# Kernel tuning notes

Measured on AMD Instinct MI355X. Metric: run time of the kernel, lower is better.

Reference implementation:

```python
import jax, jax.numpy as jnp
import numpy as np

T, D, H, E, K = 8192, 1024, 768, 16, 2


def setup_inputs() -> dict:
    key = jax.random.key(0)
    k1, k2, k3, k4, k5, k6 = jax.random.split(key, 6)
    x = jax.random.normal(k1, (T, D), dtype=jnp.float32)
    weights = jax.random.uniform(k2, (T, K), dtype=jnp.float32)
    indices = jax.random.randint(k3, (T, K), 0, E, dtype=jnp.int64)
    counts = jax.random.randint(k4, (E,), 0, 1024, dtype=jnp.int32)
    # GatedMLP params per expert: fc1: D -> 2H (value | gate), fc2: H -> D, no bias
    W1 = jax.random.normal(k5, (E, D, 2 * H), dtype=jnp.float32) * (1.0 / np.sqrt(D))
    W2 = jax.random.normal(k6, (E, H, D), dtype=jnp.float32) * (1.0 / np.sqrt(H))
    return {"x": x, "weights": weights, "indices": indices, "counts": counts, "W1": W1, "W2": W2}


def _gated_mlp(x, w1, w2):
    h = x @ w1                      # [T, 2H]
    v, g = jnp.split(h, 2, axis=-1)  # value, gate halves (torch chunk order)
    return (v * jax.nn.silu(g)) @ w2  # [T, D]


def reference(x, weights, indices, counts, W1, W2):
    # y[t] = sum_k weights[t,k] * GatedMLP_{indices[t,k]}(x[t])
    # Expressed as a masked per-expert combine: w_e[t] = sum_k weights[t,k]*[indices[t,k]==e].
    # Identical math to the torch gather/scatter loop (zero weight -> zero contribution).
    n_experts = W1.shape[0]
    y = jnp.zeros_like(x)
    for e in range(n_experts):
        w_e = jnp.sum(weights * (indices == e), axis=-1)  # [T]
        y = y + _gated_mlp(x, W1[e], W2[e]) * w_e[:, None]
    return y
```

## Files before the change

kernel.cpp:

```cpp
#include <hip/hip_runtime.h>
#include <hip/hip_bf16.h>

#define T_TOK 8192
#define D_DIM 1024
#define H_DIM 768
#define E_EXP 16
#define K_TOP 2
#define TK (T_TOK * K_TOP)
#define NT128 144
#define NT256 80

typedef __bf16 bf16x8 __attribute__((ext_vector_type(8)));
typedef unsigned short u16x8 __attribute__((ext_vector_type(8)));
typedef float f32x4 __attribute__((ext_vector_type(4)));

typedef const __attribute__((address_space(1))) void* gas_t;
typedef __attribute__((address_space(3))) void* las_t;

__device__ __forceinline__ unsigned short f2b(float f) {
    __hip_bfloat16 h = __float2bfloat16(f);
    return __builtin_bit_cast(unsigned short, h);
}
__device__ __forceinline__ float b2f(unsigned short u) {
    unsigned int x = ((unsigned int)u) << 16;
    return __builtin_bit_cast(float, x);
}

__global__ __launch_bounds__(1024) void k_route(
    const int* __restrict__ idx, const float* __restrict__ wts,
    int* __restrict__ offs, int* __restrict__ tiletab,
    int* __restrict__ rows, float* __restrict__ wslot, int* __restrict__ slot_of) {
    __shared__ int lcnt[E_EXP];
    __shared__ int lcur[E_EXP];
    const int tid = threadIdx.x;
    if (tid < E_EXP) lcnt[tid] = 0;
    __syncthreads();
    for (int i = tid; i < TK; i += 1024) atomicAdd(&lcnt[idx[i]], 1);
    __syncthreads();
    if (tid == 0) {
        int s = 0, nt = 0;
        for (int e = 0; e < E_EXP; ++e) {
            offs[e] = s;
            lcur[e] = s;
            const int n = lcnt[e];
            for (int m0 = 0; m0 < n; m0 += 128) tiletab[nt++] = (e << 16) | (m0 >> 7);
            s += n;
        }
        offs[E_EXP] = s;
        for (int i = nt; i < NT128; ++i) tiletab[i] = -1;
    }
    __syncthreads();
    for (int i = tid; i < TK; i += 1024) {
        const int e = idx[i];
        const int p = atomicAdd(&lcur[e], 1);
        rows[p] = i >> 1;
        wslot[p] = wts[i];
        slot_of[i] = p;
    }
}

#define PREP_X T_TOK
#define PREP_W1 (PREP_X + (D_DIM / 64) * ((2 * H_DIM) / 64) * E_EXP)
#define PREP_W2 (PREP_W1 + (H_DIM / 64) * (D_DIM / 64) * E_EXP)

__global__ __launch_bounds__(256) void k_prep(
    const float* __restrict__ x, const float* __restrict__ W1, const float* __restrict__ W2,
    unsigned short* __restrict__ xb, unsigned short* __restrict__ W1T,
    unsigned short* __restrict__ W2T) {
    const int b = blockIdx.x;
    const int tid = threadIdx.x;
    if (b < PREP_X) {
        const int d = tid * 4;
        const float4 v = *reinterpret_cast<const float4*>(&x[(size_t)b * D_DIM + d]);
        ushort4 u;
        u.x = f2b(v.x); u.y = f2b(v.y); u.z = f2b(v.z); u.w = f2b(v.w);
        *reinterpret_cast<ushort4*>(&xb[(size_t)b * D_DIM + d]) = u;
        return;
    }
    __shared__ float t4[64][65];
    const float* src; unsigned short* dst; int K, C, e, kb, cb, pack;
    if (b < PREP_W1) {
        const int q = b - PREP_X;
        K = D_DIM; C = 2 * H_DIM; pack = 1;
        e = q / ((K / 64) * (C / 64));
        const int r = q % ((K / 64) * (C / 64));
        kb = (r % (K / 64)) * 64; cb = (r / (K / 64)) * 64;
        src = W1; dst = W1T;
    } else {
        const int q = b - PREP_W1;
        K = H_DIM; C = D_DIM; pack = 0;
        e = q / ((K / 64) * (C / 64));
        const int r = q % ((K / 64) * (C / 64));
        kb = (r % (K / 64)) * 64; cb = (r / (K / 64)) * 64;
        src = W2; dst = W2T;
    }
    const float* s = src + ((size_t)e * K + kb) * C + cb;
#pragma unroll
    for (int i = 0; i < 4; ++i) {
        const int kk = (tid >> 4) + i * 16, c4 = (tid & 15) * 4;
        const float4 v = *reinterpret_cast<const float4*>(&s[(size_t)kk * C + c4]);
        t4[kk][c4] = v.x; t4[kk][c4 + 1] = v.y; t4[kk][c4 + 2] = v.z; t4[kk][c4 + 3] = v.w;
    }
    __syncthreads();
#pragma unroll
    for (int i = 0; i < 4; ++i) {
        const int cc = (tid >> 4) + i * 16, k4 = (tid & 15) * 4;
        const int j = cb + cc;
        int drow;
        if (pack) drow = (j < H_DIM) ? ((j >> 5) * 64 + (j & 31))
                                     : (((j - H_DIM) >> 5) * 64 + 32 + ((j - H_DIM) & 31));
        else drow = j;
        ushort4 u;
        u.x = f2b(t4[k4][cc]); u.y = f2b(t4[k4 + 1][cc]);
        u.z = f2b(t4[k4 + 2][cc]); u.w = f2b(t4[k4 + 3][cc]);
        *reinterpret_cast<ushort4*>(&dst[((size_t)e * C + drow) * K + kb + k4]) = u;
    }
}


__global__ __launch_bounds__(512, 2) void k_gemm1_fast(
    const unsigned short* __restrict__ xb, const unsigned short* __restrict__ W1T,
    const int* __restrict__ offs, const int* __restrict__ tiletab,
    const int* __restrict__ rows, unsigned short* __restrict__ act) {
    const int ti = (blockIdx.x & 7) * (NT128 / 8) + (blockIdx.x >> 3);
    const int tt = tiletab[ti];
    if (tt < 0) return;
    const int e = tt >> 16, m0 = (tt & 0xffff) << 7;
    const int off = offs[e], n_e = offs[e + 1] - off;
    const int by = blockIdx.y;

    __shared__ unsigned short SA[2][128 * 32];
    __shared__ unsigned short SB[2][256 * 32];

    const int tid = threadIdx.x;
    const int wid = tid >> 6, lane = tid & 63;
    const int l15 = lane & 15, kq = lane >> 4;
    const int wm = wid >> 2, wn = wid & 3;
    const int srow = tid >> 2;
    const int esw = (((tid & 3) ^ ((tid >> 3) & 3)) << 3);
    const int rk = ((kq ^ ((l15 >> 1) & 3)) << 3);

    int tok;
    { int s = m0 + srow; s = (s < n_e) ? s : (n_e - 1); tok = rows[off + s]; }
    size_t bB[2];
#pragma unroll
    for (int j = 0; j < 2; ++j)
        bB[j] = ((size_t)e * (2 * H_DIM) + by * 256 + j * 128 + srow) * D_DIM + esw;

    f32x4 acc[4][4];
#pragma unroll
    for (int m = 0; m < 4; ++m)
#pragma unroll
        for (int n = 0; n < 4; ++n)
#pragma unroll
            for (int r = 0; r < 4; ++r) acc[m][n][r] = 0.f;

    auto stage = [&](int buf, int k0) {
        const unsigned short* ga = xb + (size_t)tok * D_DIM + k0 + esw;
        __builtin_amdgcn_global_load_lds((gas_t)ga,
            (las_t)((char*)&SA[buf][0] + tid * 16), 16, 0, 0);
#pragma unroll
        for (int j = 0; j < 2; ++j) {
            const unsigned short* gb = W1T + bB[j] + k0;
            __builtin_amdgcn_global_load_lds((gas_t)gb,
                (las_t)((char*)&SB[buf][0] + j * 8192 + tid * 16), 16, 0, 0);
        }
    };

    stage(0, 0);
    __syncthreads();
    int c = 0;
    const int NT = D_DIM / 32;
    for (int t = 0; t < NT; ++t) {
        if (t + 1 < NT) stage(c ^ 1, (t + 1) * 32);
        bf16x8 a[4], b[4];
#pragma unroll
        for (int m = 0; m < 4; ++m) {
            const int row = wm * 64 + m * 16 + l15;
            a[m] = __builtin_bit_cast(bf16x8, *reinterpret_cast<const u16x8*>(
                &SA[c][row * 32 + rk]));
        }
#pragma unroll
        for (int n = 0; n < 4; ++n) {
            const int row = wn * 64 + n * 16 + l15;
            b[n] = __builtin_bit_cast(bf16x8, *reinterpret_cast<const u16x8*>(
                &SB[c][row * 32 + rk]));
        }
#pragma unroll
        for (int m = 0; m < 4; ++m)
#pragma unroll
            for (int n = 0; n < 4; ++n)
                acc[m][n] = __builtin_amdgcn_mfma_f32_16x16x32_bf16(a[m], b[n], acc[m][n], 0, 0, 0);
        __syncthreads();
        c ^= 1;
    }
#pragma unroll
    for (int m = 0; m < 4; ++m)
#pragma unroll
        for (int r = 0; r < 4; ++r) {
            const int row = wm * 64 + m * 16 + kq * 4 + r;
            if (m0 + row < n_e) {
#pragma unroll
                for (int nv = 0; nv < 2; ++nv) {
                    const int col = by * 128 + wn * 32 + nv * 16 + l15;
                    const float vv = acc[m][nv][r], gg = acc[m][2 + nv][r];
                    const float s = gg / (1.0f + __expf(-gg));
                    act[(size_t)(off + m0 + row) * H_DIM + col] = f2b(vv * s);
                }
            }
        }
}

__global__ __launch_bounds__(512, 2) void k_gemm2_fast(
    const unsigned short* __restrict__ act, const unsigned short* __restrict__ W2T,
    const int* __restrict__ offs, const int* __restrict__ tiletab,
    const float* __restrict__ wslot, unsigned short* __restrict__ slot_out) {
    const int ti = (blockIdx.x & 7) * (NT128 / 8) + (blockIdx.x >> 3);
    const int tt = tiletab[ti];
    if (tt < 0) return;
    const int e = tt >> 16, m0 = (tt & 0xffff) << 7;
    const int off = offs[e], n_e = offs[e + 1] - off;
    const int by = blockIdx.y;

    __shared__ unsigned short SA[2][128 * 32];
    __shared__ unsigned short SB[2][256 * 32];

    const int tid = threadIdx.x;
    const int wid = tid >> 6, lane = tid & 63;
    const int l15 = lane & 15, kq = lane >> 4;
    const int wm = wid >> 2, wn = wid & 3;
    const int srow = tid >> 2;
    const int esw = (((tid & 3) ^ ((tid >> 3) & 3)) << 3);
    const int rk = ((kq ^ ((l15 >> 1) & 3)) << 3);

    int slotA;
    { int s = m0 + srow; s = (s < n_e) ? s : (n_e - 1); slotA = off + s; }
    size_t bB[2];
#pragma unroll
    for (int j = 0; j < 2; ++j)
        bB[j] = ((size_t)e * D_DIM + by * 256 + j * 128 + srow) * H_DIM + esw;

    f32x4 acc[4][4];
#pragma unroll
    for (int m = 0; m < 4; ++m)
#pragma unroll
        for (int n = 0; n < 4; ++n)
#pragma unroll
            for (int r = 0; r < 4; ++r) acc[m][n][r] = 0.f;

    auto stage = [&](int buf, int k0) {
        const unsigned short* ga = act + (size_t)slotA * H_DIM + k0 + esw;
        __builtin_amdgcn_global_load_lds((gas_t)ga,
            (las_t)((char*)&SA[buf][0] + tid * 16), 16, 0, 0);
#pragma unroll
        for (int j = 0; j < 2; ++j) {
            const unsigned short* gb = W2T + bB[j] + k0;
            __builtin_amdgcn_global_load_lds((gas_t)gb,
                (las_t)((char*)&SB[buf][0] + j * 8192 + tid * 16), 16, 0, 0);
        }
    };

    stage(0, 0);
    __syncthreads();
    int c = 0;
    const int NT = H_DIM / 32;
    for (int t = 0; t < NT; ++t) {
        if (t + 1 < NT) stage(c ^ 1, (t + 1) * 32);
        bf16x8 a[4], b[4];
#pragma unroll
        for (int m = 0; m < 4; ++m) {
            const int row = wm * 64 + m * 16 + l15;
            a[m] = __builtin_bit_cast(bf16x8, *reinterpret_cast<const u16x8*>(
                &SA[c][row * 32 + rk]));
        }
#pragma unroll
        for (int n = 0; n < 4; ++n) {
            const int row = wn * 64 + n * 16 + l15;
            b[n] = __builtin_bit_cast(bf16x8, *reinterpret_cast<const u16x8*>(
                &SB[c][row * 32 + rk]));
        }
#pragma unroll
        for (int m = 0; m < 4; ++m)
#pragma unroll
            for (int n = 0; n < 4; ++n)
                acc[m][n] = __builtin_amdgcn_mfma_f32_16x16x32_bf16(a[m], b[n], acc[m][n], 0, 0, 0);
        __syncthreads();
        c ^= 1;
    }
#pragma unroll
    for (int m = 0; m < 4; ++m)
#pragma unroll
        for (int r = 0; r < 4; ++r) {
            const int row = wm * 64 + m * 16 + kq * 4 + r;
            if (m0 + row < n_e) {
                const int slot = off + m0 + row;
                const float w = wslot[slot];
#pragma unroll
                for (int n = 0; n < 4; ++n) {
                    const int col = by * 256 + wn * 64 + n * 16 + l15;
                    slot_out[(size_t)slot * D_DIM + col] = f2b(w * acc[m][n][r]);
                }
            }
        }
}

__global__ __launch_bounds__(256) void k_gather(const float* __restrict__ x,
                                                const int* __restrict__ rows,
                                                unsigned short* __restrict__ xg) {
    const int s = blockIdx.x, t = threadIdx.x;
    const int tok = rows[s];
    const float4 v = *reinterpret_cast<const float4*>(&x[(size_t)tok * D_DIM + t * 4]);
    ushort4 u;
    u.x = f2b(v.x); u.y = f2b(v.y); u.z = f2b(v.z); u.w = f2b(v.w);
    *reinterpret_cast<ushort4*>(&xg[(size_t)s * D_DIM + t * 4]) = u;
}

__global__ __launch_bounds__(256) void k_gemm1_fb(
    const unsigned short* __restrict__ xg, const float* __restrict__ W1,
    const int* __restrict__ offs, const int* __restrict__ tiletab,
    unsigned short* __restrict__ act) {
    const int tt = tiletab[blockIdx.x];
    if (tt < 0) return;
    const int e = tt >> 16, m0 = (tt & 0xffff) << 7;
    const int off = offs[e], n_e = offs[e + 1] - off;
    const int h0 = blockIdx.y * 64;

    __shared__ unsigned short Ab[128 * 64];
    __shared__ unsigned short Bb[128 * 66];

    const int tid = threadIdx.x;
    const int wid = tid >> 6, lane = tid & 63;
    const int l15 = lane & 15, kq = lane >> 4;

    f32x4 acc[2][8];
#pragma unroll
    for (int m = 0; m < 2; ++m)
#pragma unroll
        for (int n = 0; n < 8; ++n)
#pragma unroll
            for (int r = 0; r < 4; ++r) acc[m][n][r] = 0.f;

    for (int k0 = 0; k0 < D_DIM; k0 += 64) {
        __syncthreads();
#pragma unroll
        for (int j = 0; j < 4; ++j) {
            const int o = wid * 4096 + j * 1024 + lane * 16;
            const int row = o >> 7, kb = o & 127;
            int gr = off + m0 + row; gr = (gr < TK) ? gr : (TK - 1);
            const unsigned short* gp = xg + (size_t)gr * D_DIM + k0 + (kb >> 1);
            __builtin_amdgcn_global_load_lds((gas_t)gp,
                (las_t)((char*)Ab + wid * 4096 + j * 1024), 16, 0, 0);
        }
        {
            const float* W1e = W1 + (size_t)e * D_DIM * (2 * H_DIM);
#pragma unroll
            for (int i = 0; i < 8; ++i) {
                const int flat = tid + 256 * i;
                const int cg = flat & 31, kk = flat >> 5;
                const int cc = cg * 4;
                const int gc = (cc < 64) ? (h0 + cc) : (H_DIM + h0 + cc - 64);
                const float4 v = *reinterpret_cast<const float4*>(
                    &W1e[(size_t)(k0 + kk) * (2 * H_DIM) + gc]);
                Bb[(cc + 0) * 66 + kk] = f2b(v.x);
                Bb[(cc + 1) * 66 + kk] = f2b(v.y);
                Bb[(cc + 2) * 66 + kk] = f2b(v.z);
                Bb[(cc + 3) * 66 + kk] = f2b(v.w);
            }
        }
        __syncthreads();
#pragma unroll
        for (int ks = 0; ks < 2; ++ks) {
            bf16x8 a[2], b[8];
#pragma unroll
            for (int m = 0; m < 2; ++m)
                a[m] = __builtin_bit_cast(bf16x8, *reinterpret_cast<const u16x8*>(
                    &Ab[(wid * 32 + m * 16 + l15) * 64 + ks * 32 + kq * 8]));
#pragma unroll
            for (int n = 0; n < 8; ++n)
                b[n] = __builtin_bit_cast(bf16x8, *reinterpret_cast<const u16x8*>(
                    &Bb[(n * 16 + l15) * 66 + ks * 32 + kq * 8]));
#pragma unroll
            for (int m = 0; m < 2; ++m)
#pragma unroll
                for (int n = 0; n < 8; ++n)
                    acc[m][n] = __builtin_amdgcn_mfma_f32_16x16x32_bf16(a[m], b[n], acc[m][n], 0, 0, 0);
        }
    }
#pragma unroll
    for (int m = 0; m < 2; ++m)
#pragma unroll
        for (int n = 0; n < 4; ++n)
#pragma unroll
            for (int r = 0; r < 4; ++r) {
                const int row = wid * 32 + m * 16 + kq * 4 + r;
                if (m0 + row < n_e) {
                    const float vv = acc[m][n][r], gg = acc[m][n + 4][r];
                    const float s = gg / (1.0f + __expf(-gg));
                    act[(size_t)(off + m0 + row) * H_DIM + h0 + n * 16 + l15] = f2b(vv * s);
                }
            }
}

__global__ __launch_bounds__(256) void k_gemm2_fb(
    const unsigned short* __restrict__ act, const float* __restrict__ W2,
    const int* __restrict__ offs, const int* __restrict__ tiletab,
    const float* __restrict__ wslot, unsigned short* __restrict__ slot_out,
    float* __restrict__ y, const int* __restrict__ rows, int atomic_mode) {
    const int tt = tiletab[blockIdx.x];
    if (tt < 0) return;
    const int e = tt >> 16, m0 = (tt & 0xffff) << 7;
    const int off = offs[e], n_e = offs[e + 1] - off;
    const int n0 = blockIdx.y * 64;

    __shared__ unsigned short Ab[128 * 64];
    __shared__ unsigned short Bb[64 * 66];

    const int tid = threadIdx.x;
    const int wid = tid >> 6, lane = tid & 63;
    const int l15 = lane & 15, kq = lane >> 4;

    f32x4 acc[2][4];
#pragma unroll
    for (int m = 0; m < 2; ++m)
#pragma unroll
        for (int n = 0; n < 4; ++n)
#pragma unroll
            for (int r = 0; r < 4; ++r) acc[m][n][r] = 0.f;

    for (int k0 = 0; k0 < H_DIM; k0 += 64) {
        __syncthreads();
#pragma unroll
        for (int j = 0; j < 4; ++j) {
            const int o = wid * 4096 + j * 1024 + lane * 16;
            const int row = o >> 7, kb = o & 127;
            int gr = off + m0 + row; gr = (gr < TK) ? gr : (TK - 1);
            const unsigned short* gp = act + (size_t)gr * H_DIM + k0 + (kb >> 1);
            __builtin_amdgcn_global_load_lds((gas_t)gp,
                (las_t)((char*)Ab + wid * 4096 + j * 1024), 16, 0, 0);
        }
        {
            const float* W2e = W2 + (size_t)e * H_DIM * D_DIM;
#pragma unroll
            for (int i = 0; i < 4; ++i) {
                const int flat = tid + 256 * i;
                const int cg = flat & 15, kk = flat >> 4;
                const int cc = cg * 4;
                const float4 v = *reinterpret_cast<const float4*>(
                    &W2e[(size_t)(k0 + kk) * D_DIM + n0 + cc]);
                Bb[(cc + 0) * 66 + kk] = f2b(v.x);
                Bb[(cc + 1) * 66 + kk] = f2b(v.y);
                Bb[(cc + 2) * 66 + kk] = f2b(v.z);
                Bb[(cc + 3) * 66 + kk] = f2b(v.w);
            }
        }
        __syncthreads();
#pragma unroll
        for (int ks = 0; ks < 2; ++ks) {
            bf16x8 a[2], b[4];
#pragma unroll
            for (int m = 0; m < 2; ++m)
                a[m] = __builtin_bit_cast(bf16x8, *reinterpret_cast<const u16x8*>(
                    &Ab[(wid * 32 + m * 16 + l15) * 64 + ks * 32 + kq * 8]));
#pragma unroll
            for (int n = 0; n < 4; ++n)
                b[n] = __builtin_bit_cast(bf16x8, *reinterpret_cast<const u16x8*>(
                    &Bb[(n * 16 + l15) * 66 + ks * 32 + kq * 8]));
#pragma unroll
            for (int m = 0; m < 2; ++m)
#pragma unroll
                for (int n = 0; n < 4; ++n)
                    acc[m][n] = __builtin_amdgcn_mfma_f32_16x16x32_bf16(a[m], b[n], acc[m][n], 0, 0, 0);
        }
    }
#pragma unroll
    for (int m = 0; m < 2; ++m)
#pragma unroll
        for (int r = 0; r < 4; ++r) {
            const int row = wid * 32 + m * 16 + kq * 4 + r;
            if (m0 + row < n_e) {
                const int slot = off + m0 + row;
                const float w = wslot[slot];
#pragma unroll
                for (int n = 0; n < 4; ++n) {
                    const float o = w * acc[m][n][r];
                    if (atomic_mode)
                        atomicAdd(&y[(size_t)rows[slot] * D_DIM + n0 + n * 16 + l15], o);
                    else
                        slot_out[(size_t)slot * D_DIM + n0 + n * 16 + l15] = f2b(o);
                }
            }
        }
}

__global__ __launch_bounds__(256) void k_combine(
    const unsigned short* __restrict__ slot_out, const int* __restrict__ slot_of,
    float* __restrict__ y) {
    const int t = blockIdx.x;
    const int d = threadIdx.x * 4;
    const int s0 = slot_of[2 * t], s1 = slot_of[2 * t + 1];
    const ushort4 a = *reinterpret_cast<const ushort4*>(&slot_out[(size_t)s0 * D_DIM + d]);
    const ushort4 b = *reinterpret_cast<const ushort4*>(&slot_out[(size_t)s1 * D_DIM + d]);
    float4 r;
    r.x = b2f(a.x) + b2f(b.x);
    r.y = b2f(a.y) + b2f(b.y);
    r.z = b2f(a.z) + b2f(b.z);
    r.w = b2f(a.w) + b2f(b.w);
    *reinterpret_cast<float4*>(&y[(size_t)t * D_DIM + d]) = r;
}

extern "C" void kernel_launch(void* const* d_in, const int* in_sizes, int n_in,
                              void* d_out, int out_size, void* d_ws, size_t ws_size,
                              hipStream_t stream) {
    const float* x = (const float*)d_in[0];
    const float* wts = (const float*)d_in[1];
    const int* idx = (const int*)d_in[2];
    const float* W1 = (const float*)d_in[4];
    const float* W2 = (const float*)d_in[5];
    float* y = (float*)d_out;

    char* ws = (char*)d_ws;
    int* offs = (int*)(ws + 128);
    int* tiletab = (int*)(ws + 320);
    int* rows = (int*)(ws + 2048);
    float* wslot = (float*)(ws + 2048 + (size_t)TK * 4);
    int* slot_of = (int*)(ws + 2048 + (size_t)TK * 8);
    const size_t OFF_XG = 2048 + (size_t)TK * 12;
    unsigned short* xg = (unsigned short*)(ws + OFF_XG);
    unsigned short* xb = xg;
    const size_t OFF_ACT = OFF_XG + (size_t)TK * D_DIM * 2;
    unsigned short* act = (unsigned short*)(ws + OFF_ACT);
    const size_t OFF_SO = OFF_ACT + (size_t)TK * H_DIM * 2;
    unsigned short* slot_out = (unsigned short*)(ws + OFF_SO);
    const size_t MID_END = OFF_SO + (size_t)TK * D_DIM * 2;
    const size_t OFF_W1T = MID_END;
    unsigned short* W1T = (unsigned short*)(ws + OFF_W1T);
    const size_t OFF_W2T = OFF_W1T + (size_t)E_EXP * 2 * H_DIM * D_DIM * 2;
    unsigned short* W2T = (unsigned short*)(ws + OFF_W2T);
    const size_t FULL_END = OFF_W2T + (size_t)E_EXP * D_DIM * H_DIM * 2;

    const int full = (ws_size >= FULL_END) ? 1 : 0;
    const int atomic_mode = (!full && ws_size < MID_END) ? 1 : 0;

    k_route<<<1, 1024, 0, stream>>>(idx, wts, offs, tiletab, rows, wslot, slot_of);

    if (full) {
        k_prep<<<PREP_W2, 256, 0, stream>>>(x, W1, W2, xb, W1T, W2T);
        dim3 g1(NT128, H_DIM / 128);
        k_gemm1_fast<<<g1, 512, 0, stream>>>(xb, W1T, offs, tiletab, rows, act);
        dim3 g2(NT128, D_DIM / 256);
        k_gemm2_fast<<<g2, 512, 0, stream>>>(act, W2T, offs, tiletab, wslot, slot_out);
        k_combine<<<T_TOK, 256, 0, stream>>>(slot_out, slot_of, y);
    } else {
        k_gather<<<TK, 256, 0, stream>>>(x, rows, xg);
        dim3 g1(NT128, H_DIM / 64);
        k_gemm1_fb<<<g1, 256, 0, stream>>>(xg, W1, offs, tiletab, act);
        if (atomic_mode) hipMemsetAsync(y, 0, (size_t)out_size * 4, stream);
        dim3 g2(NT128, D_DIM / 64);
        k_gemm2_fb<<<g2, 256, 0, stream>>>(act, W2, offs, tiletab, wslot, slot_out, y, rows, atomic_mode);
        if (!atomic_mode)
            k_combine<<<T_TOK, 256, 0, stream>>>(slot_out, slot_of, y);
    }
}
```

Before: 212.2 us.

## Fuse routing into prep kernel and deepen GEMM global-to-LDS prefetch

```diff
diff --git a/kernel.cpp b/kernel.cpp
--- a/kernel.cpp
+++ b/kernel.cpp
@@ -8,7 +8,6 @@
 #define K_TOP 2
 #define TK (T_TOK * K_TOP)
 #define NT128 144
-#define NT256 80
 
 typedef __bf16 bf16x8 __attribute__((ext_vector_type(8)));
 typedef unsigned short u16x8 __attribute__((ext_vector_type(8)));
@@ -59,61 +58,97 @@
     }
 }
 
-#define PREP_X T_TOK
-#define PREP_W1 (PREP_X + (D_DIM / 64) * ((2 * H_DIM) / 64) * E_EXP)
-#define PREP_W2 (PREP_W1 + (H_DIM / 64) * (D_DIM / 64) * E_EXP)
-
-__global__ __launch_bounds__(256) void k_prep(
+#define PRB_X 2048
+#define PRB_W1 3072
+#define PRB_W2 1536
+#define PRB_TOT (1 + PRB_X + PRB_W1 + PRB_W2)
+
+__global__ __launch_bounds__(512) void k_preproute(
     const float* __restrict__ x, const float* __restrict__ W1, const float* __restrict__ W2,
+    const int* __restrict__ idx, const float* __restrict__ wts,
     unsigned short* __restrict__ xb, unsigned short* __restrict__ W1T,
-    unsigned short* __restrict__ W2T) {
+    unsigned short* __restrict__ W2T,
+    int* __restrict__ offs, int* __restrict__ tiletab,
+    int* __restrict__ rows, float* __restrict__ wslot, int* __restrict__ slot_of) {
     const int b = blockIdx.x;
     const int tid = threadIdx.x;
-    if (b < PREP_X) {
-        const int d = tid * 4;
-        const float4 v = *reinterpret_cast<const float4*>(&x[(size_t)b * D_DIM + d]);
-        ushort4 u;
-        u.x = f2b(v.x); u.y = f2b(v.y); u.z = f2b(v.z); u.w = f2b(v.w);
-        *reinterpret_cast<ushort4*>(&xb[(size_t)b * D_DIM + d]) = u;
+    if (b == 0) {
+        __shared__ int lcnt[E_EXP];
+        __shared__ int lcur[E_EXP];
+        if (tid < E_EXP) lcnt[tid] = 0;
+        __syncthreads();
+        for (int i = tid; i < TK; i += 512) atomicAdd(&lcnt[idx[i]], 1);
+        __syncthreads();
+        if (tid == 0) {
+            int s = 0, nt = 0;
+            for (int e = 0; e < E_EXP; ++e) {
+                offs[e] = s;
+                lcur[e] = s;
+                const int n = lcnt[e];
+                for (int m0 = 0; m0 < n; m0 += 128) tiletab[nt++] = (e << 16) | (m0 >> 7);
+                s += n;
+            }
+            offs[E_EXP] = s;
+            for (int i = nt; i < NT128; ++i) tiletab[i] = -1;
+        }
+        __syncthreads();
+        for (int i = tid; i < TK; i += 512) {
+            const int e = idx[i];
+            const int p = atomicAdd(&lcur[e], 1);
+            rows[p] = i >> 1;
+            wslot[p] = wts[i];
+            slot_of[i] = p;
+        }
         return;
     }
-    __shared__ float t4[64][65];
-    const float* src; unsigned short* dst; int K, C, e, kb, cb, pack;
-    if (b < PREP_W1) {
-        const int q = b - PREP_X;
+    if (b <= PRB_X) {
+        const size_t base = (size_t)(b - 1) * 4096 + (size_t)tid * 8;
+        const float4 v0 = *reinterpret_cast<const float4*>(&x[base]);
+        const float4 v1 = *reinterpret_cast<const float4*>(&x[base + 4]);
+        u16x8 u;
+        u[0] = f2b(v0.x); u[1] = f2b(v0.y); u[2] = f2b(v0.z); u[3] = f2b(v0.w);
+        u[4] = f2b(v1.x); u[5] = f2b(v1.y); u[6] = f2b(v1.z); u[7] = f2b(v1.w);
+        *reinterpret_cast<u16x8*>(&xb[base]) = u;
+        return;
+    }
+    __shared__ float t4[2][64][65];
+    const int sub = tid >> 8, t2 = tid & 255;
+    const float* src; unsigned short* dst;
+    int K, C, e, kb, cb, pack;
+    if (b <= PRB_X + PRB_W1) {
+        const int q = (b - 1 - PRB_X) * 2 + sub;
         K = D_DIM; C = 2 * H_DIM; pack = 1;
-        e = q / ((K / 64) * (C / 64));
-        const int r = q % ((K / 64) * (C / 64));
-        kb = (r % (K / 64)) * 64; cb = (r / (K / 64)) * 64;
+        e = q / 384; const int r = q % 384;
+        kb = (r % 16) * 64; cb = (r / 16) * 64;
         src = W1; dst = W1T;
     } else {
-        const int q = b - PREP_W1;
+        const int q = (b - 1 - PRB_X - PRB_W1) * 2 + sub;
         K = H_DIM; C = D_DIM; pack = 0;
-        e = q / ((K / 64) * (C / 64));
-        const int r = q % ((K / 64) * (C / 64));
-        kb = (r % (K / 64)) * 64; cb = (r / (K / 64)) * 64;
+        e = q / 192; const int r = q % 192;
+        kb = (r % 12) * 64; cb = (r / 12) * 64;
         src = W2; dst = W2T;
     }
     const float* s = src + ((size_t)e * K + kb) * C + cb;
 #pragma unroll
     for (int i = 0; i < 4; ++i) {
-        const int kk = (tid >> 4) + i * 16, c4 = (tid & 15) * 4;
+        const int kk = (t2 >> 4) + i * 16, c4 = (t2 & 15) * 4;
         const float4 v = *reinterpret_cast<const float4*>(&s[(size_t)kk * C + c4]);
-        t4[kk][c4] = v.x; t4[kk][c4 + 1] = v.y; t4[kk][c4 + 2] = v.z; t4[kk][c4 + 3] = v.w;
+        t4[sub][kk][c4] = v.x; t4[sub][kk][c4 + 1] = v.y;
+        t4[sub][kk][c4 + 2] = v.z; t4[sub][kk][c4 + 3] = v.w;
     }
     __syncthreads();
 #pragma unroll
-    for (int i = 0; i < 4; ++i) {
-        const int cc = (tid >> 4) + i * 16, k4 = (tid & 15) * 4;
+    for (int i = 0; i < 2; ++i) {
+        const int cc = (t2 >> 3) + i * 32, k8 = (t2 & 7) * 8;
         const int j = cb + cc;
         int drow;
         if (pack) drow = (j < H_DIM) ? ((j >> 5) * 64 + (j & 31))
                                      : (((j - H_DIM) >> 5) * 64 + 32 + ((j - H_DIM) & 31));
         else drow = j;
-        ushort4 u;
-        u.x = f2b(t4[k4][cc]); u.y = f2b(t4[k4 + 1][cc]);
-        u.z = f2b(t4[k4 + 2][cc]); u.w = f2b(t4[k4 + 3][cc]);
-        *reinterpret_cast<ushort4*>(&dst[((size_t)e * C + drow) * K + kb + k4]) = u;
+        u16x8 u;
+#pragma unroll
+        for (int q8 = 0; q8 < 8; ++q8) u[q8] = f2b(t4[sub][k8 + q8][cc]);
+        *reinterpret_cast<u16x8*>(&dst[((size_t)e * C + drow) * K + kb + k8]) = u;
     }
 }
 
@@ -168,11 +203,14 @@
     };
 
     stage(0, 0);
-    __syncthreads();
+    stage(1, 32);
     int c = 0;
     const int NT = D_DIM / 32;
     for (int t = 0; t < NT; ++t) {
-        if (t + 1 < NT) stage(c ^ 1, (t + 1) * 32);
+        if (t < NT - 1) asm volatile("s_waitcnt vmcnt(3)" ::: "memory");
+        else            asm volatile("s_waitcnt vmcnt(0)" ::: "memory");
+        __builtin_amdgcn_s_barrier();
+        asm volatile("" ::: "memory");
         bf16x8 a[4], b[4];
 #pragma unroll
         for (int m = 0; m < 4; ++m) {
@@ -191,7 +229,10 @@
 #pragma unroll
             for (int n = 0; n < 4; ++n)
                 acc[m][n] = __builtin_amdgcn_mfma_f32_16x16x32_bf16(a[m], b[n], acc[m][n], 0, 0, 0);
-        __syncthreads();
+        asm volatile("s_waitcnt lgkmcnt(0)" ::: "memory");
+        __builtin_amdgcn_s_barrier();
+        asm volatile("" ::: "memory");
+        if (t + 2 < NT) stage(c, (t + 2) * 32);
         c ^= 1;
     }
 #pragma unroll
@@ -261,11 +302,14 @@
     };
 
     stage(0, 0);
-    __syncthreads();
+    stage(1, 32);
     int c = 0;
     const int NT = H_DIM / 32;
     for (int t = 0; t < NT; ++t) {
-        if (t + 1 < NT) stage(c ^ 1, (t + 1) * 32);
+        if (t < NT - 1) asm volatile("s_waitcnt vmcnt(3)" ::: "memory");
+        else            asm volatile("s_waitcnt vmcnt(0)" ::: "memory");
+        __builtin_amdgcn_s_barrier();
+        asm volatile("" ::: "memory");
         bf16x8 a[4], b[4];
 #pragma unroll
         for (int m = 0; m < 4; ++m) {
@@ -284,7 +328,10 @@
 #pragma unroll
             for (int n = 0; n < 4; ++n)
                 acc[m][n] = __builtin_amdgcn_mfma_f32_16x16x32_bf16(a[m], b[n], acc[m][n], 0, 0, 0);
-        __syncthreads();
+        asm volatile("s_waitcnt lgkmcnt(0)" ::: "memory");
+        __builtin_amdgcn_s_barrier();
+        asm volatile("" ::: "memory");
+        if (t + 2 < NT) stage(c, (t + 2) * 32);
         c ^= 1;
     }
 #pragma unroll
@@ -541,16 +588,16 @@
     const int full = (ws_size >= FULL_END) ? 1 : 0;
     const int atomic_mode = (!full && ws_size < MID_END) ? 1 : 0;
 
-    k_route<<<1, 1024, 0, stream>>>(idx, wts, offs, tiletab, rows, wslot, slot_of);
-
     if (full) {
-        k_prep<<<PREP_W2, 256, 0, stream>>>(x, W1, W2, xb, W1T, W2T);
+        k_preproute<<<PRB_TOT, 512, 0, stream>>>(x, W1, W2, idx, wts, xb, W1T, W2T,
+                                                 offs, tiletab, rows, wslot, slot_of);
         dim3 g1(NT128, H_DIM / 128);
         k_gemm1_fast<<<g1, 512, 0, stream>>>(xb, W1T, offs, tiletab, rows, act);
         dim3 g2(NT128, D_DIM / 256);
         k_gemm2_fast<<<g2, 512, 0, stream>>>(act, W2T, offs, tiletab, wslot, slot_out);
         k_combine<<<T_TOK, 256, 0, stream>>>(slot_out, slot_of, y);
     } else {
+        k_route<<<1, 1024, 0, stream>>>(idx, wts, offs, tiletab, rows, wslot, slot_of);
         k_gather<<<TK, 256, 0, stream>>>(x, rows, xg);
         dim3 g1(NT128, H_DIM / 64);
         k_gemm1_fb<<<g1, 256, 0, stream>>>(xg, W1, offs, tiletab, act);
```

New measurement: 208.9 us. About the same (-1.5%).
